# Kernel tuning notes

Measured on AMD Instinct MI355X. Metric: run time of the kernel, lower is better.

The kernel has to match this reference:

```python
import jax, jax.numpy as jnp
import numpy as np

EPS = 1e-5  # BatchNorm eps


def _conv3x3(x, w, b):
    # x: [B,C,H,W], w: [O,C,3,3], b: [O]
    y = jax.lax.conv_general_dilated(
        x, w, window_strides=(1, 1), padding=((1, 1), (1, 1)),
        dimension_numbers=("NCHW", "OIHW", "NCHW"))
    return y + b[None, :, None, None]


def _bilinear_gather(x, py, px):
    """Bilinear sample x at fractional coords (zero outside bounds).
    x: [B,C,H,W]; py, px: [B,K,H,W] -> returns [B,C,K,H,W]."""
    B, C, H, W = x.shape
    K = py.shape[1]
    x_flat = x.reshape(B, C, H * W)
    y0 = jnp.floor(py)
    x0 = jnp.floor(px)
    wy1 = py - y0
    wx1 = px - x0
    wy0 = 1.0 - wy1
    wx0 = 1.0 - wx1

    def gather(yi, xi):
        valid = (yi >= 0) & (yi <= H - 1) & (xi >= 0) & (xi <= W - 1)
        yc = jnp.clip(yi, 0, H - 1).astype(jnp.int32)
        xc = jnp.clip(xi, 0, W - 1).astype(jnp.int32)
        idx = (yc * W + xc).reshape(B, 1, K * H * W)
        g = jnp.take_along_axis(x_flat, idx, axis=2).reshape(B, C, K, H, W)
        return g * valid.astype(x.dtype)[:, None]

    val = (gather(y0, x0) * (wy0 * wx0)[:, None]
           + gather(y0, x0 + 1.0) * (wy0 * wx1)[:, None]
           + gather(y0 + 1.0, x0) * (wy1 * wx0)[:, None]
           + gather(y0 + 1.0, x0 + 1.0) * (wy1 * wx1)[:, None])
    return val


def _deform_conv_bn_relu(x, w_off, b_off, w_dcn, b_dcn, gamma, beta):
    B, Ci, H, W = x.shape
    Co = w_dcn.shape[0]
    # offset/mask branch: 27 = 9 dy | 9 dx (cat, then interpreted interleaved) | 9 mask
    om = _conv3x3(x, w_off, b_off)                       # [B,27,H,W]
    offset = jnp.concatenate([om[:, :9], om[:, 9:18]], axis=1)  # [B,18,H,W]
    mask = jax.nn.sigmoid(om[:, 18:27])                  # [B,9,H,W]
    dy = offset[:, 0::2]                                 # [B,9,H,W]
    dx = offset[:, 1::2]                                 # [B,9,H,W]
    # base sampling grid: stride 1, pad 1, dilation 1, 3x3 kernel
    ky = jnp.repeat(jnp.arange(3, dtype=x.dtype), 3)     # [9]
    kx = jnp.tile(jnp.arange(3, dtype=x.dtype), 3)       # [9]
    hh = jnp.arange(H, dtype=x.dtype)
    ww = jnp.arange(W, dtype=x.dtype)
    py = dy + (hh - 1.0)[None, None, :, None] + ky[None, :, None, None]
    px = dx + (ww - 1.0)[None, None, None, :] + kx[None, :, None, None]
    sampled = _bilinear_gather(x, py, px)                # [B,Ci,9,H,W]
    sampled = sampled * mask[:, None]                    # modulated (DCNv2)
    out = jnp.einsum('bckhw,ock->bohw', sampled, w_dcn.reshape(Co, Ci, 9))
    out = out + b_dcn[None, :, None, None]
    # BatchNorm2d (training mode: batch statistics, biased variance) + ReLU
    mean = jnp.mean(out, axis=(0, 2, 3), keepdims=True)
    var = jnp.mean(jnp.square(out - mean), axis=(0, 2, 3), keepdims=True)
    bn = (out - mean) * jax.lax.rsqrt(var + EPS)
    bn = bn * gamma[None, :, None, None] + beta[None, :, None, None]
    return jax.nn.relu(bn)


def setup_inputs() -> dict:
    key = jax.random.key(0)
    k0, k1, k2 = jax.random.split(key, 3)
    B, Ci, Co, H, W = 2, 256, 256, 96, 96
    x = jax.random.normal(k0, (B, Ci, H, W), jnp.float32)
    # small offset-conv weights -> offsets within a few pixels (realistic after training)
    w_off = jax.random.normal(k1, (27, Ci, 3, 3), jnp.float32) * 0.01
    b_off = jnp.zeros((27,), jnp.float32)
    w_dcn = jax.random.normal(k2, (Co, Ci, 3, 3), jnp.float32) * (1.0 / np.sqrt(Ci * 9))
    b_dcn = jnp.zeros((Co,), jnp.float32)
    gamma = jnp.ones((Co,), jnp.float32)
    beta = jnp.zeros((Co,), jnp.float32)
    return {"x": x, "w_off": w_off, "b_off": b_off, "w_dcn": w_dcn,
            "b_dcn": b_dcn, "gamma": gamma, "beta": beta}


def reference(x, w_off, b_off, w_dcn, b_dcn, gamma, beta):
    return _deform_conv_bn_relu(x, w_off, b_off, w_dcn, b_dcn, gamma, beta)
```

## Files before the change

### kernel.cpp

```cpp
#include <hip/hip_runtime.h>


typedef unsigned short ushort_t;
typedef unsigned int uint_t;
typedef __attribute__((ext_vector_type(8))) short bf16x8;
typedef __attribute__((ext_vector_type(4))) float f32x4;
typedef __attribute__((ext_vector_type(2), aligned(4))) float f32x2a;

#define HH 96
#define WW 96
#define HWSZ 9216
#define CI 256
#define CO 256
#define NB 2
#define NPIX 18432
#define KTOT 2304

__device__ __forceinline__ ushort_t f2bf(float f) {
  unsigned int u = __float_as_uint(f);
  u += 0x7fffu + ((u >> 16) & 1u);
  return (ushort_t)(u >> 16);
}
__device__ __forceinline__ float u2f(uint_t u) { return __uint_as_float(u); }

__device__ __forceinline__ void gload16(const void* g, void* l) {
  __builtin_amdgcn_global_load_lds(
      (const __attribute__((address_space(1))) unsigned int*)g,
      (__attribute__((address_space(3))) unsigned int*)l, 16, 0, 0);
}

__global__ void cvt_w9(const float* __restrict__ w, ushort_t* __restrict__ o) {
  int i = blockIdx.x * 256 + threadIdx.x;
  int oo = i / KTOT;
  int kk = i - oo * KTOT;
  o[(kk >> 3) * 2048 + oo * 8 + (kk & 7)] = f2bf(w[i]);
}

__global__ void cvt_woff9(const float* __restrict__ w, ushort_t* __restrict__ o) {
  int i = blockIdx.x * 256 + threadIdx.x;
  int m = i / KTOT;
  int kk = i - m * KTOT;
  float v = (m < 27) ? w[m * KTOT + kk] : 0.f;
  o[(kk >> 3) * 256 + m * 8 + (kk & 7)] = f2bf(v);
}

__global__ __launch_bounds__(512, 2) void off_gemm(
    const float* __restrict__ x, const ushort_t* __restrict__ w27r,
    float* __restrict__ om_part) {
  __shared__ __align__(16) ushort_t A27[2][2048];
  __shared__ __align__(16) ushort_t B64[4096];
  __shared__ uint2 tbl[9][64];

  const int tid = threadIdx.x;
  const int lane = tid & 63, wid = tid >> 6;
  const int p0 = blockIdx.x * 64;
  const int part = blockIdx.y;
  const int bimg = p0 / HWSZ;
  const int hw0 = p0 - bimg * HWSZ;
  const float* xb = x + (size_t)bimg * CI * HWSZ;

  for (int e = tid; e < 576; e += 512) {
    int k = e >> 6, px = e & 63;
    int hw = hw0 + px, h = hw / WW, w_ = hw - h * WW;
    int dy = k / 3 - 1, dx = k % 3 - 1;
    bool ok = (h + dy >= 0) && (h + dy < HH) && (w_ + dx >= 0) && (w_ + dx < WW);
    tbl[k][px] = make_uint2(ok ? (uint_t)(hw + dy * WW + dx) : 0u,
                            ok ? 0x3f800000u : 0u);
  }

  const int lg = lane >> 4, lm = lane & 15;
  const int wr = wid >> 2, wc = wid & 3;
  f32x4 acc = (f32x4){0.f, 0.f, 0.f, 0.f};

  int cj[8], kj[8];
#pragma unroll
  for (int j = 0; j < 8; ++j) {
    int kk = part * 1152 + wid * 8 + j;
    cj[j] = kk / 9;
    kj[j] = kk - 9 * cj[j];
  }
  __syncthreads();

  float rv0[8], rm0[8], rv1[8], rm1[8];
  const int k0 = part * 18;

#define OG_RAW(RV, RM)                                                        \
  { _Pragma("unroll") for (int j = 0; j < 8; ++j) {                           \
      uint2 e_ = tbl[kj[j]][lane];                                            \
      RV[j] = xb[cj[j] * HWSZ + (int)e_.x];                                   \
      RM[j] = u2f(e_.y);                                                      \
      kj[j] += 1; cj[j] += 7;                                                 \
      if (kj[j] == 9) { kj[j] = 0; cj[j] += 1; } } }
#define OG_GA(CH, BUF)                                                        \
  gload16(w27r + (size_t)(CH) * 2048 + (tid & 255) * 8, &A27[BUF][(wid & 3) * 512]);
#define OG_STEP(CUR, RVC, RMC, RVN, RMN, KO)                                  \
  {                                                                           \
    if ((KO) < 17) {                                                          \
      OG_RAW(RVN, RMN)                                                        \
      OG_GA(k0 + (KO) + 1, (CUR) ^ 1)                                         \
      asm volatile("s_waitcnt vmcnt(10)" ::: "memory");                       \
    } else {                                                                  \
      asm volatile("s_waitcnt vmcnt(1)" ::: "memory");                        \
    }                                                                         \
    __builtin_amdgcn_sched_barrier(0);                                        \
    {                                                                         \
      ushort_t sv_[8] __attribute__((aligned(16)));                           \
      _Pragma("unroll") for (int j = 0; j < 8; ++j)                           \
        sv_[j] = f2bf(RVC[j] * RMC[j]);                                       \
      *(uint4*)&B64[tid * 8] = *(const uint4*)sv_;                            \
    }                                                                         \
    if ((KO) < 17) asm volatile("s_waitcnt vmcnt(9) lgkmcnt(0)" ::: "memory"); \
    else           asm volatile("s_waitcnt vmcnt(0) lgkmcnt(0)" ::: "memory"); \
    __builtin_amdgcn_s_barrier();                                             \
    __builtin_amdgcn_sched_barrier(0);                                        \
    _Pragma("unroll") for (int s = 0; s < 2; ++s) {                           \
      bf16x8 af = *(const bf16x8*)&A27[CUR][((s * 4 + lg) * 32 + wr * 16 + lm) * 8]; \
      bf16x8 bfv = *(const bf16x8*)&B64[((s * 4 + lg) * 64 + wc * 16 + lm) * 8];     \
      acc = __builtin_amdgcn_mfma_f32_16x16x32_bf16(af, bfv, acc, 0, 0, 0);   \
    }                                                                         \
    asm volatile("s_waitcnt lgkmcnt(0)" ::: "memory");                        \
    __builtin_amdgcn_s_barrier();                                             \
    __builtin_amdgcn_sched_barrier(0);                                        \
  }

  OG_RAW(rv0, rm0)
  OG_GA(k0, 0)
  for (int ko2 = 0; ko2 < 9; ++ko2) {
    const int ko = ko2 * 2;
    OG_STEP(0, rv0, rm0, rv1, rm1, ko)
    OG_STEP(1, rv1, rm1, rv0, rm0, ko + 1)
  }
#undef OG_RAW
#undef OG_GA
#undef OG_STEP

  int row = wr * 16 + lg * 4;
  int col = p0 + wc * 16 + lm;
#pragma unroll
  for (int r = 0; r < 4; ++r)
    if (row + r < 27)
      om_part[((size_t)(part * 27 + row + r)) * NPIX + col] = acc[r];
}

__global__ void prep_kernel(const float* __restrict__ om_part, const float* __restrict__ b_off,
                            uint_t* __restrict__ offs, float4* __restrict__ wts) {
  int n = blockIdx.x * 128 + threadIdx.x;
  float omv[27];
#pragma unroll
  for (int ch = 0; ch < 27; ++ch)
    omv[ch] = b_off[ch] + om_part[(size_t)ch * NPIX + n] +
              om_part[((size_t)(27 + ch)) * NPIX + n];
  int hw = n % HWSZ;
  int h = hw / WW, w = hw - h * WW;
#pragma unroll
  for (int k = 0; k < 9; ++k) {
    float dy = omv[2 * k], dx = omv[2 * k + 1];
    float mk = 1.f / (1.f + __expf(-omv[18 + k]));
    float py = dy + (float)(h - 1 + k / 3);
    float px = dx + (float)(w - 1 + k % 3);
    float y0f = floorf(py), x0f = floorf(px);
    int y0 = (int)y0f, x0 = (int)x0f;
    float wy1 = py - y0f, wx1 = px - x0f;
    float wy0 = 1.f - wy1, wx0 = 1.f - wx1;
    float vy0 = (y0 >= 0 && y0 <= HH - 1) ? 1.f : 0.f;
    float vy1 = (y0 + 1 >= 0 && y0 + 1 <= HH - 1) ? 1.f : 0.f;
    int yc0 = min(max(y0, 0), HH - 1), yc1 = min(max(y0 + 1, 0), HH - 1);
    int xa = min(max(x0, 0), WW - 2);
    float a_, b_;
    if (x0 >= 0 && x0 <= WW - 2)      { a_ = wx0; b_ = wx1; }
    else if (x0 == -1)                { a_ = wx1; b_ = 0.f; }
    else if (x0 == WW - 1)            { a_ = 0.f; b_ = wx0; }
    else                              { a_ = 0.f; b_ = 0.f; }
    float s0 = mk * vy0 * wy0, s1 = mk * vy1 * wy1;
    offs[(size_t)k * NPIX + n] = (uint_t)(yc0 * WW + xa) | ((uint_t)(yc1 * WW + xa) << 16);
    wts[(size_t)k * NPIX + n] = make_float4(a_ * s0, b_ * s0, a_ * s1, b_ * s1);
  }
}

__global__ __launch_bounds__(512, 2) void sample_lds(
    const float* __restrict__ x, const uint_t* __restrict__ offs,
    const float4* __restrict__ wts, ushort_t* __restrict__ S_g) {
  __shared__ float xl[2][HWSZ];
  const int tid = threadIdx.x;
  const int wid = tid >> 6;
  const int img = blockIdx.x >> 1;
  const int half = blockIdx.x & 1;
  const int cp = blockIdx.y;
  const int n0 = img * HWSZ + half * 4608;

  {
    const float* src = x + ((size_t)(img * CI + 2 * cp)) * HWSZ;
    float* dst = &xl[0][0];
#pragma unroll
    for (int i = 0; i < 9; ++i)
      gload16(src + i * 2048 + tid * 4, dst + i * 2048 + wid * 256);
  }
  __syncthreads();

  for (int j = 0; j < 9; ++j) {
    const int n = n0 + tid + j * 512;
    uint_t ofr[9]; float4 wtr[9];
#pragma unroll
    for (int k = 0; k < 9; ++k) {
      ofr[k] = offs[(size_t)k * NPIX + n];
      wtr[k] = wts[(size_t)k * NPIX + n];
    }
    uint_t pkw[9];
#pragma unroll
    for (int i = 0; i < 9; ++i) pkw[i] = 0u;
#pragma unroll
    for (int k = 0; k < 9; ++k) {
      const int o0 = (int)(ofr[k] & 0xffffu);
      const int o1 = (int)(ofr[k] >> 16);
      float a0x = xl[0][o0], a0y = xl[0][o0 + 1];
      float b0x = xl[0][o1], b0y = xl[0][o1 + 1];
      float a1x = xl[1][o0], a1y = xl[1][o0 + 1];
      float b1x = xl[1][o1], b1y = xl[1][o1 + 1];
      float v0 = wtr[k].x * a0x + wtr[k].y * a0y + wtr[k].z * b0x + wtr[k].w * b0y;
      float v1 = wtr[k].x * a1x + wtr[k].y * a1y + wtr[k].z * b1x + wtr[k].w * b1y;
      const int q0 = k, q1 = 9 + k;
      pkw[q0 >> 1] |= ((uint_t)f2bf(v0)) << ((q0 & 1) * 16);
      pkw[q1 >> 1] |= ((uint_t)f2bf(v1)) << ((q1 & 1) * 16);
    }
#pragma unroll
    for (int jj = 0; jj < 9; ++jj) {
      const int kk = cp * 18 + 2 * jj;
      *(uint_t*)&S_g[((size_t)(kk >> 3) * NPIX + n) * 8 + (kk & 7)] = pkw[jj];
    }
  }
}

__global__ __launch_bounds__(512, 2) void s_gemm(
    const ushort_t* __restrict__ w9r, const ushort_t* __restrict__ S_g,
    const float* __restrict__ b_dcn, float* __restrict__ out) {
  __shared__ __align__(16) ushort_t A[4][8192];
  __shared__ __align__(16) ushort_t S[4][2048];

  const int tid = threadIdx.x;
  const int lane = tid & 63, wid = tid >> 6;
  const int p0 = blockIdx.x * 64;
  const int bimg = p0 / HWSZ;
  const int hw0 = p0 - bimg * HWSZ;
  const int lg = lane >> 4, lm = lane & 15;
  const int wr = wid >> 1, wc = wid & 1;

  f32x4 acc[4][2];
#pragma unroll
  for (int i = 0; i < 4; ++i)
#pragma unroll
    for (int j = 0; j < 2; ++j) acc[i][j] = (f32x4){0.f, 0.f, 0.f, 0.f};

#define SG_STAGE(CH, BUF)                                                     \
  {                                                                           \
    gload16(w9r + (size_t)(CH) * 8192 + tid * 8, &A[BUF][wid * 512]);         \
    gload16(w9r + (size_t)(CH) * 8192 + 4096 + tid * 8, &A[BUF][4096 + wid * 512]); \
    if (wid < 4)                                                              \
      gload16(S_g + ((size_t)((CH) * 4 + wid) * NPIX + p0 + lane) * 8,        \
              &S[BUF][wid * 512]);                                            \
  }
#define SG_MFMA(BUF)                                                          \
  {                                                                           \
    bf16x8 bfr0 = *(const bf16x8*)&S[BUF][(lg * 64 + wc * 32 + lm) * 8];      \
    bf16x8 bfr1 = *(const bf16x8*)&S[BUF][(lg * 64 + wc * 32 + 16 + lm) * 8]; \
    _Pragma("unroll") for (int mi = 0; mi < 4; ++mi) {                        \
      bf16x8 af = *(const bf16x8*)&A[BUF][(lg * 256 + wr * 64 + mi * 16 + lm) * 8]; \
      acc[mi][0] = __builtin_amdgcn_mfma_f32_16x16x32_bf16(af, bfr0, acc[mi][0], 0, 0, 0); \
      acc[mi][1] = __builtin_amdgcn_mfma_f32_16x16x32_bf16(af, bfr1, acc[mi][1], 0, 0, 0); \
    }                                                                         \
  }

  SG_STAGE(0, 0)
  SG_STAGE(1, 1)
  for (int ko = 0; ko < 70; ++ko) {
    SG_STAGE(ko + 2, (ko + 2) & 3)
    if (wid < 4) { asm volatile("s_waitcnt vmcnt(6)" ::: "memory"); }
    else         { asm volatile("s_waitcnt vmcnt(4)" ::: "memory"); }
    __builtin_amdgcn_s_barrier();
    __builtin_amdgcn_sched_barrier(0);
    SG_MFMA(ko & 3)
  }
  if (wid < 4) { asm volatile("s_waitcnt vmcnt(3)" ::: "memory"); }
  else         { asm volatile("s_waitcnt vmcnt(2)" ::: "memory"); }
  __builtin_amdgcn_s_barrier();
  __builtin_amdgcn_sched_barrier(0);
  SG_MFMA(2)
  asm volatile("s_waitcnt vmcnt(0)" ::: "memory");
  __builtin_amdgcn_s_barrier();
  __builtin_amdgcn_sched_barrier(0);
  SG_MFMA(3)
#undef SG_STAGE
#undef SG_MFMA

  const int hwv0 = hw0 + wc * 32 + lm;
#pragma unroll
  for (int mi = 0; mi < 4; ++mi) {
    int obase = wr * 64 + mi * 16 + lg * 4;
#pragma unroll
    for (int ni = 0; ni < 2; ++ni)
#pragma unroll
      for (int r = 0; r < 4; ++r) {
        int o = obase + r;
        out[((size_t)(bimg * CO + o)) * HWSZ + hwv0 + ni * 16] = acc[mi][ni][r] + b_dcn[o];
      }
  }
}

__global__ __launch_bounds__(256) void bn_stats1(const float* __restrict__ out,
                                                 float2* __restrict__ part) {
  int o = blockIdx.x, s = blockIdx.y, tid = threadIdx.x;
  const float4* p = (const float4*)(out + ((size_t)((s >> 1) * CO + o)) * HWSZ + (s & 1) * 4608);
  float sum = 0.f, sq = 0.f;
#pragma unroll
  for (int j = tid; j < 1152; j += 256) {
    float4 v = p[j];
    sum += v.x + v.y + v.z + v.w;
    sq += v.x * v.x + v.y * v.y + v.z * v.z + v.w * v.w;
  }
#pragma unroll
  for (int off = 32; off > 0; off >>= 1) {
    sum += __shfl_xor(sum, off);
    sq += __shfl_xor(sq, off);
  }
  __shared__ float rs[4], rq[4];
  if ((tid & 63) == 0) { rs[tid >> 6] = sum; rq[tid >> 6] = sq; }
  __syncthreads();
  if (tid == 0)
    part[o * 4 + s] = make_float2(rs[0] + rs[1] + rs[2] + rs[3],
                                  rq[0] + rq[1] + rq[2] + rq[3]);
}

__global__ __launch_bounds__(256) void bn_finl(const float2* __restrict__ part,
                                               const float* __restrict__ gamma,
                                               const float* __restrict__ beta,
                                               float* __restrict__ ss) {
  int o = threadIdx.x;
  float s = 0.f, sq = 0.f;
#pragma unroll
  for (int i = 0; i < 4; ++i) {
    float2 p = part[o * 4 + i];
    s += p.x; sq += p.y;
  }
  float mean = s * (1.f / (float)NPIX);
  float var = sq * (1.f / (float)NPIX) - mean * mean;
  float rstd = rsqrtf(var + 1e-5f);
  float sc = rstd * gamma[o];
  ss[o] = sc;
  ss[CO + o] = beta[o] - mean * sc;
}

__global__ void bn_apply(float* __restrict__ out, const float* __restrict__ ss) {
  int i = blockIdx.x * 256 + threadIdx.x;
  float4 v = ((float4*)out)[i];
  int o = (i / (HWSZ / 4)) & 255;
  float sc = ss[o], sh = ss[CO + o];
  v.x = fmaxf(v.x * sc + sh, 0.f);
  v.y = fmaxf(v.y * sc + sh, 0.f);
  v.z = fmaxf(v.z * sc + sh, 0.f);
  v.w = fmaxf(v.w * sc + sh, 0.f);
  ((float4*)out)[i] = v;
}

extern "C" void kernel_launch(void* const* d_in, const int* in_sizes, int n_in,
                              void* d_out, int out_size, void* d_ws, size_t ws_size,
                              hipStream_t stream) {
  const float* x = (const float*)d_in[0];
  const float* w_off = (const float*)d_in[1];
  const float* b_off = (const float*)d_in[2];
  const float* w_dcn = (const float*)d_in[3];
  const float* b_dcn = (const float*)d_in[4];
  const float* gamma = (const float*)d_in[5];
  const float* beta = (const float*)d_in[6];
  float* out = (float*)d_out;

  char* ws = (char*)d_ws;

  size_t base = 84934656;
  ushort_t* S_g   = (ushort_t*)(ws);
  float*    om    = (float*)(ws + base);
  uint_t*   offs  = (uint_t*)(ws + base + 3981312);
  float4*   wts   = (float4*)(ws + base + 4644864);
  ushort_t* w9r   = (ushort_t*)(ws + base + 7299072);
  ushort_t* w27r  = (ushort_t*)(ws + base + 8478720);
  float*    ss    = (float*)(ws + base + 8626176);
  float2*   bnp   = (float2*)(ws + base + 8628224);

  cvt_w9<<<(CO * KTOT) / 256, 256, 0, stream>>>(w_dcn, w9r);
  cvt_woff9<<<(32 * KTOT) / 256, 256, 0, stream>>>(w_off, w27r);
  off_gemm<<<dim3(NPIX / 64, 2), 512, 0, stream>>>(x, w27r, om);
  prep_kernel<<<NPIX / 128, 128, 0, stream>>>(om, b_off, offs, wts);
  sample_lds<<<dim3(4, 128), 512, 0, stream>>>(x, offs, wts, S_g);
  s_gemm<<<NPIX / 64, 512, 0, stream>>>(w9r, S_g, b_dcn, out);
  bn_stats1<<<dim3(CO, 4), 256, 0, stream>>>(out, bnp);
  bn_finl<<<1, 256, 0, stream>>>(bnp, gamma, beta, ss);
  bn_apply<<<(out_size / 4) / 256, 256, 0, stream>>>(out, ss);
}
```

Before: 147.2 us.

## Fuse BN statistics into GEMM epilogue and interleave channel pairs in LDS

The GEMM epilogue now computes per-channel partial sums and sums of squares, reduces them with shuffles and LDS, and writes one partial per block. This removes the separate bn_stats kernel and its full re-read of the output. bn_finl now serially reduces 288 partials per channel, which adds a small serial tail. Separately, sample_lds stores the two input channels interleaved in LDS so each bilinear tap is one 8-byte read instead of two scalar reads, at the cost of replacing async global-to-LDS loads with register-staged loads.

```diff
diff --git a/kernel.cpp b/kernel.cpp
--- a/kernel.cpp
+++ b/kernel.cpp
@@ -6,6 +6,7 @@
 typedef __attribute__((ext_vector_type(8))) short bf16x8;
 typedef __attribute__((ext_vector_type(4))) float f32x4;
 typedef __attribute__((ext_vector_type(2), aligned(4))) float f32x2a;
+typedef __attribute__((ext_vector_type(2))) float f32x2v;
 
 #define HH 96
 #define WW 96
@@ -180,20 +181,23 @@
 __global__ __launch_bounds__(512, 2) void sample_lds(
     const float* __restrict__ x, const uint_t* __restrict__ offs,
     const float4* __restrict__ wts, ushort_t* __restrict__ S_g) {
-  __shared__ float xl[2][HWSZ];
+  __shared__ __align__(16) float xl2[HWSZ * 2];
   const int tid = threadIdx.x;
-  const int wid = tid >> 6;
   const int img = blockIdx.x >> 1;
   const int half = blockIdx.x & 1;
   const int cp = blockIdx.y;
   const int n0 = img * HWSZ + half * 4608;
 
   {
-    const float* src = x + ((size_t)(img * CI + 2 * cp)) * HWSZ;
-    float* dst = &xl[0][0];
-#pragma unroll
-    for (int i = 0; i < 9; ++i)
-      gload16(src + i * 2048 + tid * 4, dst + i * 2048 + wid * 256);
+    const float* s0 = x + ((size_t)(img * CI + 2 * cp)) * HWSZ;
+    const float* s1 = s0 + HWSZ;
+#pragma unroll
+    for (int i = 0; i < 9; ++i) {
+      int col = i * 1024 + tid * 2;
+      f32x2v c0 = *(const f32x2v*)(s0 + col);
+      f32x2v c1 = *(const f32x2v*)(s1 + col);
+      *(float4*)&xl2[col * 2] = make_float4(c0[0], c1[0], c0[1], c1[1]);
+    }
   }
   __syncthreads();
 
@@ -212,12 +216,12 @@
     for (int k = 0; k < 9; ++k) {
       const int o0 = (int)(ofr[k] & 0xffffu);
       const int o1 = (int)(ofr[k] >> 16);
-      float a0x = xl[0][o0], a0y = xl[0][o0 + 1];
-      float b0x = xl[0][o1], b0y = xl[0][o1 + 1];
-      float a1x = xl[1][o0], a1y = xl[1][o0 + 1];
-      float b1x = xl[1][o1], b1y = xl[1][o1 + 1];
-      float v0 = wtr[k].x * a0x + wtr[k].y * a0y + wtr[k].z * b0x + wtr[k].w * b0y;
-      float v1 = wtr[k].x * a1x + wtr[k].y * a1y + wtr[k].z * b1x + wtr[k].w * b1y;
+      f32x2v pa0 = *(const f32x2v*)&xl2[o0 * 2];
+      f32x2v pa1 = *(const f32x2v*)&xl2[o0 * 2 + 2];
+      f32x2v pb0 = *(const f32x2v*)&xl2[o1 * 2];
+      f32x2v pb1 = *(const f32x2v*)&xl2[o1 * 2 + 2];
+      float v0 = wtr[k].x * pa0[0] + wtr[k].y * pa1[0] + wtr[k].z * pb0[0] + wtr[k].w * pb1[0];
+      float v1 = wtr[k].x * pa0[1] + wtr[k].y * pa1[1] + wtr[k].z * pb0[1] + wtr[k].w * pb1[1];
       const int q0 = k, q1 = 9 + k;
       pkw[q0 >> 1] |= ((uint_t)f2bf(v0)) << ((q0 & 1) * 16);
       pkw[q1 >> 1] |= ((uint_t)f2bf(v1)) << ((q1 & 1) * 16);
@@ -232,7 +236,8 @@
 
 __global__ __launch_bounds__(512, 2) void s_gemm(
     const ushort_t* __restrict__ w9r, const ushort_t* __restrict__ S_g,
-    const float* __restrict__ b_dcn, float* __restrict__ out) {
+    const float* __restrict__ b_dcn, float* __restrict__ out,
+    float2* __restrict__ bnp2) {
   __shared__ __align__(16) ushort_t A[4][8192];
   __shared__ __align__(16) ushort_t S[4][2048];
 
@@ -292,56 +297,60 @@
 #undef SG_MFMA
 
   const int hwv0 = hw0 + wc * 32 + lm;
+  float bsum[16], bsq[16];
 #pragma unroll
   for (int mi = 0; mi < 4; ++mi) {
-    int obase = wr * 64 + mi * 16 + lg * 4;
-#pragma unroll
-    for (int ni = 0; ni < 2; ++ni)
-#pragma unroll
-      for (int r = 0; r < 4; ++r) {
-        int o = obase + r;
-        out[((size_t)(bimg * CO + o)) * HWSZ + hwv0 + ni * 16] = acc[mi][ni][r] + b_dcn[o];
-      }
-  }
-}
-
-__global__ __launch_bounds__(256) void bn_stats1(const float* __restrict__ out,
-                                                 float2* __restrict__ part) {
-  int o = blockIdx.x, s = blockIdx.y, tid = threadIdx.x;
-  const float4* p = (const float4*)(out + ((size_t)((s >> 1) * CO + o)) * HWSZ + (s & 1) * 4608);
-  float sum = 0.f, sq = 0.f;
-#pragma unroll
-  for (int j = tid; j < 1152; j += 256) {
-    float4 v = p[j];
-    sum += v.x + v.y + v.z + v.w;
-    sq += v.x * v.x + v.y * v.y + v.z * v.z + v.w * v.w;
-  }
-#pragma unroll
-  for (int off = 32; off > 0; off >>= 1) {
-    sum += __shfl_xor(sum, off);
-    sq += __shfl_xor(sq, off);
-  }
-  __shared__ float rs[4], rq[4];
-  if ((tid & 63) == 0) { rs[tid >> 6] = sum; rq[tid >> 6] = sq; }
+#pragma unroll
+    for (int r = 0; r < 4; ++r) {
+      int o = wr * 64 + mi * 16 + lg * 4 + r;
+      float b = b_dcn[o];
+      float v0 = acc[mi][0][r] + b;
+      float v1 = acc[mi][1][r] + b;
+      out[((size_t)(bimg * CO + o)) * HWSZ + hwv0] = v0;
+      out[((size_t)(bimg * CO + o)) * HWSZ + hwv0 + 16] = v1;
+      bsum[mi * 4 + r] = v0 + v1;
+      bsq[mi * 4 + r] = v0 * v0 + v1 * v1;
+    }
+  }
+#pragma unroll
+  for (int d = 1; d < 16; d <<= 1) {
+#pragma unroll
+    for (int i = 0; i < 16; ++i) {
+      bsum[i] += __shfl_xor(bsum[i], d);
+      bsq[i] += __shfl_xor(bsq[i], d);
+    }
+  }
+  asm volatile("s_waitcnt lgkmcnt(0)" ::: "memory");
+  __builtin_amdgcn_s_barrier();
+  float* red = (float*)&A[0][0];
+  if (lm == 0) {
+#pragma unroll
+    for (int i = 0; i < 16; ++i) {
+      int o = wr * 64 + (i >> 2) * 16 + lg * 4 + (i & 3);
+      red[o * 2 + wc] = bsum[i];
+      red[512 + o * 2 + wc] = bsq[i];
+    }
+  }
   __syncthreads();
-  if (tid == 0)
-    part[o * 4 + s] = make_float2(rs[0] + rs[1] + rs[2] + rs[3],
-                                  rq[0] + rq[1] + rq[2] + rq[3]);
-}
-
-__global__ __launch_bounds__(256) void bn_finl(const float2* __restrict__ part,
+  if (tid < 256) {
+    float s = red[tid * 2] + red[tid * 2 + 1];
+    float q = red[512 + tid * 2] + red[512 + tid * 2 + 1];
+    bnp2[(size_t)tid * 288 + blockIdx.x] = make_float2(s, q);
+  }
+}
+
+__global__ __launch_bounds__(256) void bn_finl(const float2* __restrict__ bnp2,
                                                const float* __restrict__ gamma,
                                                const float* __restrict__ beta,
                                                float* __restrict__ ss) {
   int o = threadIdx.x;
-  float s = 0.f, sq = 0.f;
-#pragma unroll
-  for (int i = 0; i < 4; ++i) {
-    float2 p = part[o * 4 + i];
-    s += p.x; sq += p.y;
+  float s = 0.f, q = 0.f;
+  for (int j = 0; j < 288; ++j) {
+    float2 p = bnp2[(size_t)o * 288 + j];
+    s += p.x; q += p.y;
   }
   float mean = s * (1.f / (float)NPIX);
-  float var = sq * (1.f / (float)NPIX) - mean * mean;
+  float var = q * (1.f / (float)NPIX) - mean * mean;
   float rstd = rsqrtf(var + 1e-5f);
   float sc = rstd * gamma[o];
   ss[o] = sc;
@@ -377,20 +386,19 @@
   size_t base = 84934656;
   ushort_t* S_g   = (ushort_t*)(ws);
   float*    om    = (float*)(ws + base);
+  float2*   bnp2  = (float2*)(ws + base);
   uint_t*   offs  = (uint_t*)(ws + base + 3981312);
   float4*   wts   = (float4*)(ws + base + 4644864);
   ushort_t* w9r   = (ushort_t*)(ws + base + 7299072);
   ushort_t* w27r  = (ushort_t*)(ws + base + 8478720);
   float*    ss    = (float*)(ws + base + 8626176);
-  float2*   bnp   = (float2*)(ws + base + 8628224);
 
   cvt_w9<<<(CO * KTOT) / 256, 256, 0, stream>>>(w_dcn, w9r);
   cvt_woff9<<<(32 * KTOT) / 256, 256, 0, stream>>>(w_off, w27r);
   off_gemm<<<dim3(NPIX / 64, 2), 512, 0, stream>>>(x, w27r, om);
   prep_kernel<<<NPIX / 128, 128, 0, stream>>>(om, b_off, offs, wts);
   sample_lds<<<dim3(4, 128), 512, 0, stream>>>(x, offs, wts, S_g);
-  s_gemm<<<NPIX / 64, 512, 0, stream>>>(w9r, S_g, b_dcn, out);
-  bn_stats1<<<dim3(CO, 4), 256, 0, stream>>>(out, bnp);
-  bn_finl<<<1, 256, 0, stream>>>(bnp, gamma, beta, ss);
+  s_gemm<<<NPIX / 64, 512, 0, stream>>>(w9r, S_g, b_dcn, out, bnp2);
+  bn_finl<<<1, 256, 0, stream>>>(bnp2, gamma, beta, ss);
   bn_apply<<<(out_size / 4) / 256, 256, 0, stream>>>(out, ss);
 }
```

Measured after the change: 161.2 us. 9.5% more time.
